# Optimization experiments

Measured on AMD Instinct MI355X. Metric: run time of the kernel, lower is better.

## Reference

```python
import jax, jax.numpy as jnp
import numpy as np

B, S, D_IN, D_ST = 4, 4096, 1024, 1024


def setup_inputs() -> dict:
    key = jax.random.key(0)
    ks = jax.random.split(key, 7)
    s_in = 1.0 / np.sqrt(D_IN)
    s_st = 1.0 / np.sqrt(D_ST)
    return {
        "x": jax.random.normal(ks[0], (B, S, D_IN), dtype=jnp.float32),
        "gate_w": jax.random.uniform(ks[1], (D_IN, D_ST), jnp.float32, -s_in, s_in),
        "gate_b": jax.random.uniform(ks[2], (D_ST,), jnp.float32, -s_in, s_in),
        "inp_w": jax.random.uniform(ks[3], (D_IN, D_ST), jnp.float32, -s_in, s_in),
        "inp_b": jax.random.uniform(ks[4], (D_ST,), jnp.float32, -s_in, s_in),
        "out_w": jax.random.uniform(ks[5], (D_ST, D_IN), jnp.float32, -s_st, s_st),
        "out_b": jax.random.uniform(ks[6], (D_IN,), jnp.float32, -s_st, s_st),
    }


def reference(x, gate_w, gate_b, inp_w, inp_b, out_w, out_b):
    # x: [B, S, D_in]
    inp = jnp.einsum("bsd,de->bse", x, inp_w) + inp_b      # [B,S,Dst]
    gate = jax.nn.sigmoid(jnp.einsum("bsd,de->bse", x, gate_w) + gate_b)
    b_t = (1.0 - gate) * inp                               # [B,S,Dst]

    # affine recurrence h_t = gate_t * h_{t-1} + b_t via lax.scan over time
    def step(h, ab):
        a, b = ab
        h = a * h + b
        return h, h

    a_sb = jnp.swapaxes(gate, 0, 1)  # [S,B,Dst]
    b_sb = jnp.swapaxes(b_t, 0, 1)
    h0 = jnp.zeros((x.shape[0], inp.shape[-1]), dtype=x.dtype)
    _, hs = jax.lax.scan(step, h0, (a_sb, b_sb))           # [S,B,Dst]
    scan_out = jnp.swapaxes(hs, 0, 1)                      # [B,S,Dst]

    return x + jnp.einsum("bse,ed->bsd", scan_out, out_w) + out_b
```

## Files before the change

### kernel.cpp

```cpp
#include <hip/hip_runtime.h>

typedef unsigned short u16;
typedef unsigned int   u32;
typedef __bf16 bf16x8 __attribute__((ext_vector_type(8)));
typedef float  f32x4  __attribute__((ext_vector_type(4)));

#define DEVI __device__ __forceinline__

DEVI u16 f2bf(float f) {
    union { float f; u32 u; } c; c.f = f;
    u32 u = c.u;
    u32 r = (u + 0x7fffu + ((u >> 16) & 1u)) >> 16;
    return (u16)r;
}
DEVI float bf2f(u16 v) {
    union { u32 u; float f; } c; c.u = ((u32)v) << 16;
    return c.f;
}

DEVI void gload16(const void* g, void* l) {
    __builtin_amdgcn_global_load_lds(
        (const __attribute__((address_space(1))) void*)g,
        (__attribute__((address_space(3))) void*)l, 16, 0, 0);
}


#define SP1     __builtin_amdgcn_s_setprio(1)
#define SP0     __builtin_amdgcn_s_setprio(0)

DEVI void stage_half(const u16* g, u16* slot, int tid) {
    const int r = tid >> 3;
    const int ks = (((tid & 7) ^ (r & 7)) << 3);
    gload16(g + (long)r * 1024 + ks, slot + tid * 8);
    gload16(g + (long)(r + 64) * 1024 + ks, slot + 4096 + tid * 8);
}

DEVI f32x4 mfma(const bf16x8& a, const bf16x8& b, const f32x4& c) {
    return __builtin_amdgcn_mfma_f32_16x16x32_bf16(a, b, c, 0, 0, 0);
}

#define PH2(Q, MB, READB, STG, GATE)                                         \
    {                                                                        \
        if (READB) {                                                         \
            _Pragma("unroll")                                                \
            for (int n = 0; n < 4; ++n) {                                    \
                bh[n][0] = *(const bf16x8*)(lds + (Q) + bbase + n * 1024 + kA); \
                bh[n][1] = *(const bf16x8*)(lds + (Q) + bbase + n * 1024 + kB); \
            }                                                                \
        }                                                                    \
        bf16x8 a0k0 = *(const bf16x8*)(lds + (Q) + abase + (MB) * 2048 + kA); \
        bf16x8 a0k1 = *(const bf16x8*)(lds + (Q) + abase + (MB) * 2048 + kB); \
        bf16x8 a1k0 = *(const bf16x8*)(lds + (Q) + abase + (MB) * 2048 + 1024 + kA); \
        bf16x8 a1k1 = *(const bf16x8*)(lds + (Q) + abase + (MB) * 2048 + 1024 + kB); \
        STG;                                                                 \
        SP1;                                                                 \
        _Pragma("unroll")                                                    \
        for (int n = 0; n < 4; ++n) {                                        \
            acc[(MB) * 2][n]     = mfma(a0k0, bh[n][0], acc[(MB) * 2][n]);   \
            acc[(MB) * 2][n]     = mfma(a0k1, bh[n][1], acc[(MB) * 2][n]);   \
            acc[(MB) * 2 + 1][n] = mfma(a1k0, bh[n][0], acc[(MB) * 2 + 1][n]); \
            acc[(MB) * 2 + 1][n] = mfma(a1k1, bh[n][1], acc[(MB) * 2 + 1][n]); \
        }                                                                    \
        {                                                                    \
            const int M2 = (MB) + 1;                                         \
            bf16x8 c0k0 = *(const bf16x8*)(lds + (Q) + abase + M2 * 2048 + kA); \
            bf16x8 c0k1 = *(const bf16x8*)(lds + (Q) + abase + M2 * 2048 + kB); \
            bf16x8 c1k0 = *(const bf16x8*)(lds + (Q) + abase + M2 * 2048 + 1024 + kA); \
            bf16x8 c1k1 = *(const bf16x8*)(lds + (Q) + abase + M2 * 2048 + 1024 + kB); \
            _Pragma("unroll")                                                \
            for (int n = 0; n < 4; ++n) {                                    \
                acc[M2 * 2][n]     = mfma(c0k0, bh[n][0], acc[M2 * 2][n]);   \
                acc[M2 * 2][n]     = mfma(c0k1, bh[n][1], acc[M2 * 2][n]);   \
                acc[M2 * 2 + 1][n] = mfma(c1k0, bh[n][0], acc[M2 * 2 + 1][n]); \
                acc[M2 * 2 + 1][n] = mfma(c1k1, bh[n][1], acc[M2 * 2 + 1][n]); \
            }                                                                \
        }                                                                    \
        SP0;                                                                 \
        GATE;                                                                \
    }

#define NOP do {} while (0)
#define TCLOSE { __syncthreads(); }
#define AH(t, h) (Ab + (long)(h) * 131072 + (t) * 64)
#define BH(t, h) (Bb + (long)(h) * 131072 + (t) * 64)

DEVI void pipe256(const u16* Ab, const u16* Bb, u16* lds,
                  f32x4 (&acc)[8][4], int tid) {
    const int lane = tid & 63;
    const int wm = (tid >> 6) >> 2, wn = (tid >> 6) & 3;
    const int kA = (((lane >> 4) ^ (lane & 7)) << 3);
    const int kB = kA ^ 32;
    const int abase = wm * 8192 + (lane & 15) * 64;
    const int bbase = 16384 + (wn >> 1) * 8192 + ((wn & 1) * 64 + (lane & 15)) * 64;

    stage_half(AH(0, 0), lds + 0,     tid);
    stage_half(AH(0, 1), lds + 8192,  tid);
    stage_half(BH(0, 0), lds + 16384, tid);
    stage_half(BH(0, 1), lds + 24576, tid);
    __syncthreads();

    bf16x8 bh[4][2];

#pragma unroll 1
    for (int j = 0; j < 7; ++j) {
        const int T = 2 * j;
        PH2(0, 0, 1,
            { stage_half(AH(T + 1, 0), lds + 32768, tid);
              stage_half(AH(T + 1, 1), lds + 32768 + 8192, tid); }, NOP);
        PH2(0, 2, 0,
            { stage_half(BH(T + 1, 0), lds + 32768 + 16384, tid);
              stage_half(BH(T + 1, 1), lds + 32768 + 24576, tid); }, TCLOSE);
        PH2(32768, 0, 1,
            { stage_half(AH(T + 2, 0), lds + 0, tid);
              stage_half(AH(T + 2, 1), lds + 8192, tid); }, NOP);
        PH2(32768, 2, 0,
            { stage_half(BH(T + 2, 0), lds + 16384, tid);
              stage_half(BH(T + 2, 1), lds + 24576, tid); }, TCLOSE);
    }
    PH2(0, 0, 1,
        { stage_half(AH(15, 0), lds + 32768, tid);
          stage_half(AH(15, 1), lds + 32768 + 8192, tid); }, NOP);
    PH2(0, 2, 0,
        { stage_half(BH(15, 0), lds + 32768 + 16384, tid);
          stage_half(BH(15, 1), lds + 32768 + 24576, tid); }, TCLOSE);
    PH2(32768, 0, 1, NOP, NOP);
    PH2(32768, 2, 0, NOP, NOP);
}


__global__ __launch_bounds__(512, 1) void k_gemm_cat8(
    const u16* __restrict__ A, const u16* __restrict__ Bcat,
    const float* __restrict__ gb, const float* __restrict__ ib,
    u32* __restrict__ ab, float2* __restrict__ cAB) {
    __shared__ __align__(16) u16 lds[65536];
    const int tid = threadIdx.x, lane = tid & 63;
    const int wm = (tid >> 6) >> 2, wn = (tid >> 6) & 3;

    int fid = (int)blockIdx.y * 8 + (int)blockIdx.x;
    int swz = (fid & 7) * 64 + (fid >> 3);
    const long bn = swz & 7, bm = swz >> 3;

    f32x4 acc[8][4] = {};
    pipe256(A + bm * 256 * 1024, Bcat + bn * 256 * 1024, lds, acc, tid);

    const long rbase = bm * 256 + wm * 128;
    const int chbase = (int)bn * 128 + wn * 32;
    float sA[2][8], sB[2][8];
#pragma unroll
    for (int t = 0; t < 2; ++t) {
        int ch = chbase + t * 16 + (lane & 15);
        float g0 = gb[ch], i0 = ib[ch];
#pragma unroll
        for (int m = 0; m < 8; ++m) {
            long row = rbase + m * 16 + ((lane >> 4) << 2);
            float Aseg = 1.0f, Bseg = 0.0f;
#pragma unroll
            for (int i = 0; i < 4; ++i) {
                float pg = acc[m][2 * t][i] + g0;
                float pi = acc[m][2 * t + 1][i] + i0;
                float aa = 1.0f / (1.0f + __expf(-pg));
                float bb = (1.0f - aa) * pi;
                u16 au = f2bf(aa), bu = f2bf(bb);
                ab[(row + i) * 1024 + ch] = (u32)au | ((u32)bu << 16);
                float ar = bf2f(au), br = bf2f(bu);
                Aseg = ar * Aseg;
                Bseg = ar * Bseg + br;
            }
            sA[t][m] = Aseg;
            sB[t][m] = Bseg;
        }
    }
#pragma unroll
    for (int t = 0; t < 2; ++t) {
#pragma unroll
        for (int c2 = 0; c2 < 2; ++c2) {
            float Ac = 1.0f, Bc = 0.0f;
#pragma unroll
            for (int mm = 0; mm < 4; ++mm) {
                int m = c2 * 4 + mm;
#pragma unroll
                for (int q = 0; q < 4; ++q) {
                    float Aq = __shfl(sA[t][m], (lane & 15) + q * 16);
                    float Bq = __shfl(sB[t][m], (lane & 15) + q * 16);
                    Ac = Aq * Ac;
                    Bc = Aq * Bc + Bq;
                }
            }
            if ((lane >> 4) == 0) {
                long gc = (rbase >> 6) + c2;
                int ch = chbase + t * 16 + (lane & 15);
                cAB[gc * 1024 + ch] = make_float2(Ac, Bc);
            }
        }
    }
}


__global__ __launch_bounds__(512, 1) void k_gemm_out8(
    const u16* __restrict__ A, const u16* __restrict__ Bt,
    const u16* __restrict__ xbf, const float* __restrict__ ob,
    float* __restrict__ out) {
    __shared__ __align__(16) u16 lds[65536];
    const int tid = threadIdx.x, lane = tid & 63;
    const int wm = (tid >> 6) >> 2, wn = (tid >> 6) & 3;

    int fid = (int)blockIdx.y * 4 + (int)blockIdx.x;
    int swz = (fid & 7) * 32 + (fid >> 3);
    const long bn = swz & 3, bm = swz >> 2;

    f32x4 acc[8][4] = {};
    pipe256(A + bm * 256 * 1024, Bt + bn * 256 * 1024, lds, acc, tid);

    const long rbase = bm * 256 + wm * 128;
    const int cbase = (int)bn * 256 + wn * 64;
#pragma unroll
    for (int n = 0; n < 4; ++n) {
        int col = cbase + n * 16 + (lane & 15);
        float o0 = ob[col];
#pragma unroll
        for (int m = 0; m < 8; ++m) {
            long row = rbase + m * 16 + ((lane >> 4) << 2);
#pragma unroll
            for (int i = 0; i < 4; ++i) {
                long o = (row + i) * 1024 + col;
                out[o] = acc[m][n][i] + o0 + bf2f(xbf[o]);
            }
        }
    }
}


__global__ __launch_bounds__(256) void k_prep(
    const float4* __restrict__ x4, uint2* __restrict__ xb2,
    const float* __restrict__ gw, const float* __restrict__ iw,
    u16* __restrict__ catW, const float* __restrict__ ow,
    u16* __restrict__ owT) {
    __shared__ float t[32][33];
    int bid = blockIdx.x;
    if (bid < 16384) {
        int i = bid * 256 + threadIdx.x;
        float4 v = x4[i];
        uint2 r;
        r.x = (u32)f2bf(v.x) | ((u32)f2bf(v.y) << 16);
        r.y = (u32)f2bf(v.z) | ((u32)f2bf(v.w) << 16);
        xb2[i] = r;
        return;
    }
    int xi = threadIdx.x & 31, y = threadIdx.x >> 5;
    if (bid < 18432) {
        int q = bid - 16384;
        int c0 = (q & 31) * 32, r0 = ((q >> 5) & 31) * 32, z = q >> 10;
        const float* w = z ? iw : gw;
        for (int i = y; i < 32; i += 8) t[i][xi] = w[(size_t)(r0 + i) * 1024 + c0 + xi];
        __syncthreads();
        for (int i = y; i < 32; i += 8) {
            int ch = c0 + i;
            int r = ((ch >> 4) << 5) | (z << 4) | (ch & 15);
            catW[(size_t)r * 1024 + r0 + xi] = f2bf(t[xi][i]);
        }
    } else {
        int q = bid - 18432;
        int c0 = (q & 31) * 32, r0 = (q >> 5) * 32;
        for (int i = y; i < 32; i += 8) t[i][xi] = ow[(size_t)(r0 + i) * 1024 + c0 + xi];
        __syncthreads();
        for (int i = y; i < 32; i += 8)
            owT[(size_t)(c0 + i) * 1024 + r0 + xi] = f2bf(t[xi][i]);
    }
}


__global__ __launch_bounds__(256) void k_scanB(const float2* __restrict__ cAB,
                                               float* __restrict__ hin) {
    int e = blockIdx.x * 256 + threadIdx.x;
    int bt = blockIdx.y;
    float H = 0.f;
#pragma unroll
    for (int c = 0; c < 64; ++c) {
        long s = ((long)bt * 64 + c) * 1024 + e;
        hin[s] = H;
        float2 v = cAB[s];
        H = v.x * H + v.y;
    }
}

__global__ __launch_bounds__(256) void k_scanC(const u32* __restrict__ ab,
                                               const float* __restrict__ hin,
                                               u16* __restrict__ hout) {
    int e = blockIdx.x * 256 + threadIdx.x;
    int c = blockIdx.y, bt = blockIdx.z;
    long base = ((long)bt * 4096 + c * 64) * 1024 + e;
    float H = hin[((long)bt * 64 + c) * 1024 + e];
#pragma unroll 4
    for (int i = 0; i < 64; ++i) {
        u32 v = ab[base + (long)i * 1024];
        H = bf2f((u16)v) * H + bf2f((u16)(v >> 16));
        hout[base + (long)i * 1024] = f2bf(H);
    }
}


extern "C" void kernel_launch(void* const* d_in, const int* in_sizes, int n_in,
                              void* d_out, int out_size, void* d_ws, size_t ws_size,
                              hipStream_t stream) {
    const float* x      = (const float*)d_in[0];
    const float* gate_w = (const float*)d_in[1];
    const float* gate_b = (const float*)d_in[2];
    const float* inp_w  = (const float*)d_in[3];
    const float* inp_b  = (const float*)d_in[4];
    const float* out_w  = (const float*)d_in[5];
    const float* out_b  = (const float*)d_in[6];
    float* out = (float*)d_out;

    const int Bsz = 4, S = 4096, Din = 1024, Dst = 1024;
    const int M = Bsz * S;

    char* w = (char*)d_ws;
    u16* xb      = (u16*)(w);
    u16* catW    = (u16*)(w + 33554432);
    u16* owT     = (u16*)(w + 37748736);
    u16* hbf     = (u16*)(w + 39845888);
    float2* cAB  = (float2*)(w + 73400320);
    float* hin   = (float*)(w + 75497472);

    u32* ab = (u32*)d_out;

    k_prep<<<19456, 256, 0, stream>>>((const float4*)x, (uint2*)xb,
                                      gate_w, inp_w, catW, out_w, owT);

    k_gemm_cat8<<<dim3(8, M / 256), 512, 0, stream>>>(xb, catW, gate_b, inp_b, ab, cAB);

    k_scanB<<<dim3(4, Bsz), 256, 0, stream>>>(cAB, hin);
    k_scanC<<<dim3(4, 64, Bsz), 256, 0, stream>>>(ab, hin, hbf);

    k_gemm_out8<<<dim3(4, M / 256), 512, 0, stream>>>(hbf, owT, xb, out_b, out);
}
```

Baseline: 165.5 us.

## Shrink GEMM tiles to 128x128 with 4 waves and two blocks per CU

Both GEMM kernels move from 256x256 tiles with 8 waves and one block per CU to 128x128 tiles with 4 waves and a launch bound of two blocks per CU. The LDS buffers are halved and the fine-grained phase interleaving is replaced by a simpler whole-tile double buffer. The grid becomes four times larger, which is meant to improve occupancy and wave balance and to let two resident blocks overlap each other's latency. In exchange each tile reuses its operands less, so more data is loaded from global memory and L2, and the carefully tuned intra-block pipelining is lost.

After: 162.4 us, median of 2. Within noise of the previous version (-1.9%).

```diff
diff --git a/kernel.cpp b/kernel.cpp
--- a/kernel.cpp
+++ b/kernel.cpp
@@ -28,130 +28,99 @@
 #define SP1     __builtin_amdgcn_s_setprio(1)
 #define SP0     __builtin_amdgcn_s_setprio(0)
 
-DEVI void stage_half(const u16* g, u16* slot, int tid) {
-    const int r = tid >> 3;
-    const int ks = (((tid & 7) ^ (r & 7)) << 3);
-    gload16(g + (long)r * 1024 + ks, slot + tid * 8);
-    gload16(g + (long)(r + 64) * 1024 + ks, slot + 4096 + tid * 8);
+DEVI void stage128(const u16* g, u16* slot, int tid) {
+    const int ks = (((tid & 7) ^ ((tid >> 3) & 7)) << 3);
+#pragma unroll
+    for (int j = 0; j < 4; ++j) {
+        const int r = j * 32 + (tid >> 3);
+        gload16(g + (long)r * 1024 + ks, slot + j * 2048 + tid * 8);
+    }
 }
 
 DEVI f32x4 mfma(const bf16x8& a, const bf16x8& b, const f32x4& c) {
     return __builtin_amdgcn_mfma_f32_16x16x32_bf16(a, b, c, 0, 0, 0);
 }
 
-#define PH2(Q, MB, READB, STG, GATE)                                         \
+#define NOP do {} while (0)
+#define TCLOSE { __syncthreads(); }
+
+#define TILE(Q, STG, SYNC)                                                   \
     {                                                                        \
-        if (READB) {                                                         \
+        STG;                                                                 \
+        bf16x8 bh0[4], bh1[4], aa0[4], aa1[4];                               \
+        _Pragma("unroll")                                                    \
+        for (int n = 0; n < 4; ++n) {                                        \
+            bh0[n] = *(const bf16x8*)(lds + (Q) + bbase + n * 1024 + kA);    \
+            bh1[n] = *(const bf16x8*)(lds + (Q) + bbase + n * 1024 + kB);    \
+        }                                                                    \
+        _Pragma("unroll")                                                    \
+        for (int m = 0; m < 4; ++m) {                                        \
+            aa0[m] = *(const bf16x8*)(lds + (Q) + abase + m * 1024 + kA);    \
+            aa1[m] = *(const bf16x8*)(lds + (Q) + abase + m * 1024 + kB);    \
+        }                                                                    \
+        SP1;                                                                 \
+        _Pragma("unroll")                                                    \
+        for (int m = 0; m < 4; ++m) {                                        \
             _Pragma("unroll")                                                \
             for (int n = 0; n < 4; ++n) {                                    \
-                bh[n][0] = *(const bf16x8*)(lds + (Q) + bbase + n * 1024 + kA); \
-                bh[n][1] = *(const bf16x8*)(lds + (Q) + bbase + n * 1024 + kB); \
-            }                                                                \
-        }                                                                    \
-        bf16x8 a0k0 = *(const bf16x8*)(lds + (Q) + abase + (MB) * 2048 + kA); \
-        bf16x8 a0k1 = *(const bf16x8*)(lds + (Q) + abase + (MB) * 2048 + kB); \
-        bf16x8 a1k0 = *(const bf16x8*)(lds + (Q) + abase + (MB) * 2048 + 1024 + kA); \
-        bf16x8 a1k1 = *(const bf16x8*)(lds + (Q) + abase + (MB) * 2048 + 1024 + kB); \
-        STG;                                                                 \
-        SP1;                                                                 \
-        _Pragma("unroll")                                                    \
-        for (int n = 0; n < 4; ++n) {                                        \
-            acc[(MB) * 2][n]     = mfma(a0k0, bh[n][0], acc[(MB) * 2][n]);   \
-            acc[(MB) * 2][n]     = mfma(a0k1, bh[n][1], acc[(MB) * 2][n]);   \
-            acc[(MB) * 2 + 1][n] = mfma(a1k0, bh[n][0], acc[(MB) * 2 + 1][n]); \
-            acc[(MB) * 2 + 1][n] = mfma(a1k1, bh[n][1], acc[(MB) * 2 + 1][n]); \
-        }                                                                    \
-        {                                                                    \
-            const int M2 = (MB) + 1;                                         \
-            bf16x8 c0k0 = *(const bf16x8*)(lds + (Q) + abase + M2 * 2048 + kA); \
-            bf16x8 c0k1 = *(const bf16x8*)(lds + (Q) + abase + M2 * 2048 + kB); \
-            bf16x8 c1k0 = *(const bf16x8*)(lds + (Q) + abase + M2 * 2048 + 1024 + kA); \
-            bf16x8 c1k1 = *(const bf16x8*)(lds + (Q) + abase + M2 * 2048 + 1024 + kB); \
-            _Pragma("unroll")                                                \
-            for (int n = 0; n < 4; ++n) {                                    \
-                acc[M2 * 2][n]     = mfma(c0k0, bh[n][0], acc[M2 * 2][n]);   \
-                acc[M2 * 2][n]     = mfma(c0k1, bh[n][1], acc[M2 * 2][n]);   \
-                acc[M2 * 2 + 1][n] = mfma(c1k0, bh[n][0], acc[M2 * 2 + 1][n]); \
-                acc[M2 * 2 + 1][n] = mfma(c1k1, bh[n][1], acc[M2 * 2 + 1][n]); \
+                acc[m][n] = mfma(aa0[m], bh0[n], acc[m][n]);                 \
+                acc[m][n] = mfma(aa1[m], bh1[n], acc[m][n]);                 \
             }                                                                \
         }                                                                    \
         SP0;                                                                 \
-        GATE;                                                                \
-    }
-
-#define NOP do {} while (0)
-#define TCLOSE { __syncthreads(); }
-#define AH(t, h) (Ab + (long)(h) * 131072 + (t) * 64)
-#define BH(t, h) (Bb + (long)(h) * 131072 + (t) * 64)
-
-DEVI void pipe256(const u16* Ab, const u16* Bb, u16* lds,
-                  f32x4 (&acc)[8][4], int tid) {
+        SYNC;                                                                \
+    }
+
+#define STA(t, buf) stage128(Ab + (t) * 64, lds + (buf), tid)
+#define STB(t, buf) stage128(Bb + (t) * 64, lds + (buf) + 8192, tid)
+
+DEVI void pipe128(const u16* Ab, const u16* Bb, u16* lds,
+                  f32x4 (&acc)[4][4], int tid) {
     const int lane = tid & 63;
-    const int wm = (tid >> 6) >> 2, wn = (tid >> 6) & 3;
+    const int wm = (tid >> 6) >> 1, wn = (tid >> 6) & 1;
     const int kA = (((lane >> 4) ^ (lane & 7)) << 3);
     const int kB = kA ^ 32;
-    const int abase = wm * 8192 + (lane & 15) * 64;
-    const int bbase = 16384 + (wn >> 1) * 8192 + ((wn & 1) * 64 + (lane & 15)) * 64;
-
-    stage_half(AH(0, 0), lds + 0,     tid);
-    stage_half(AH(0, 1), lds + 8192,  tid);
-    stage_half(BH(0, 0), lds + 16384, tid);
-    stage_half(BH(0, 1), lds + 24576, tid);
+    const int abase = wm * 4096 + (lane & 15) * 64;
+    const int bbase = 8192 + wn * 4096 + (lane & 15) * 64;
+
+    STA(0, 0); STB(0, 0);
     __syncthreads();
-
-    bf16x8 bh[4][2];
 
 #pragma unroll 1
     for (int j = 0; j < 7; ++j) {
         const int T = 2 * j;
-        PH2(0, 0, 1,
-            { stage_half(AH(T + 1, 0), lds + 32768, tid);
-              stage_half(AH(T + 1, 1), lds + 32768 + 8192, tid); }, NOP);
-        PH2(0, 2, 0,
-            { stage_half(BH(T + 1, 0), lds + 32768 + 16384, tid);
-              stage_half(BH(T + 1, 1), lds + 32768 + 24576, tid); }, TCLOSE);
-        PH2(32768, 0, 1,
-            { stage_half(AH(T + 2, 0), lds + 0, tid);
-              stage_half(AH(T + 2, 1), lds + 8192, tid); }, NOP);
-        PH2(32768, 2, 0,
-            { stage_half(BH(T + 2, 0), lds + 16384, tid);
-              stage_half(BH(T + 2, 1), lds + 24576, tid); }, TCLOSE);
-    }
-    PH2(0, 0, 1,
-        { stage_half(AH(15, 0), lds + 32768, tid);
-          stage_half(AH(15, 1), lds + 32768 + 8192, tid); }, NOP);
-    PH2(0, 2, 0,
-        { stage_half(BH(15, 0), lds + 32768 + 16384, tid);
-          stage_half(BH(15, 1), lds + 32768 + 24576, tid); }, TCLOSE);
-    PH2(32768, 0, 1, NOP, NOP);
-    PH2(32768, 2, 0, NOP, NOP);
-}
-
-
-__global__ __launch_bounds__(512, 1) void k_gemm_cat8(
+        TILE(0,     { STA(T + 1, 16384); STB(T + 1, 16384); }, TCLOSE);
+        TILE(16384, { STA(T + 2, 0);     STB(T + 2, 0);     }, TCLOSE);
+    }
+    TILE(0,     { STA(15, 16384); STB(15, 16384); }, TCLOSE);
+    TILE(16384, NOP, NOP);
+}
+
+
+__global__ __launch_bounds__(256, 2) void k_gemm_cat8(
     const u16* __restrict__ A, const u16* __restrict__ Bcat,
     const float* __restrict__ gb, const float* __restrict__ ib,
     u32* __restrict__ ab, float2* __restrict__ cAB) {
-    __shared__ __align__(16) u16 lds[65536];
+    __shared__ __align__(16) u16 lds[32768];
     const int tid = threadIdx.x, lane = tid & 63;
-    const int wm = (tid >> 6) >> 2, wn = (tid >> 6) & 3;
-
-    int fid = (int)blockIdx.y * 8 + (int)blockIdx.x;
-    int swz = (fid & 7) * 64 + (fid >> 3);
-    const long bn = swz & 7, bm = swz >> 3;
-
-    f32x4 acc[8][4] = {};
-    pipe256(A + bm * 256 * 1024, Bcat + bn * 256 * 1024, lds, acc, tid);
-
-    const long rbase = bm * 256 + wm * 128;
-    const int chbase = (int)bn * 128 + wn * 32;
-    float sA[2][8], sB[2][8];
+    const int wm = (tid >> 6) >> 1, wn = (tid >> 6) & 1;
+
+    int fid = (int)blockIdx.y * 16 + (int)blockIdx.x;
+    int swz = (fid & 7) * 256 + (fid >> 3);
+    const long bn = swz & 15, bm = swz >> 4;
+
+    f32x4 acc[4][4] = {};
+    pipe128(A + bm * 128 * 1024, Bcat + bn * 128 * 1024, lds, acc, tid);
+
+    const long rbase = bm * 128 + wm * 64;
+    const int chbase = (int)bn * 64 + wn * 32;
+    float sA[2][4], sB[2][4];
 #pragma unroll
     for (int t = 0; t < 2; ++t) {
         int ch = chbase + t * 16 + (lane & 15);
         float g0 = gb[ch], i0 = ib[ch];
 #pragma unroll
-        for (int m = 0; m < 8; ++m) {
+        for (int m = 0; m < 4; ++m) {
             long row = rbase + m * 16 + ((lane >> 4) << 2);
             float Aseg = 1.0f, Bseg = 0.0f;
 #pragma unroll
@@ -172,53 +141,49 @@
     }
 #pragma unroll
     for (int t = 0; t < 2; ++t) {
-#pragma unroll
-        for (int c2 = 0; c2 < 2; ++c2) {
-            float Ac = 1.0f, Bc = 0.0f;
-#pragma unroll
-            for (int mm = 0; mm < 4; ++mm) {
-                int m = c2 * 4 + mm;
-#pragma unroll
-                for (int q = 0; q < 4; ++q) {
-                    float Aq = __shfl(sA[t][m], (lane & 15) + q * 16);
-                    float Bq = __shfl(sB[t][m], (lane & 15) + q * 16);
-                    Ac = Aq * Ac;
-                    Bc = Aq * Bc + Bq;
-                }
+        float Ac = 1.0f, Bc = 0.0f;
+#pragma unroll
+        for (int m = 0; m < 4; ++m) {
+#pragma unroll
+            for (int q = 0; q < 4; ++q) {
+                float Aq = __shfl(sA[t][m], (lane & 15) + q * 16);
+                float Bq = __shfl(sB[t][m], (lane & 15) + q * 16);
+                Ac = Aq * Ac;
+                Bc = Aq * Bc + Bq;
             }
-            if ((lane >> 4) == 0) {
-                long gc = (rbase >> 6) + c2;
-                int ch = chbase + t * 16 + (lane & 15);
-                cAB[gc * 1024 + ch] = make_float2(Ac, Bc);
-            }
-        }
-    }
-}
-
-
-__global__ __launch_bounds__(512, 1) void k_gemm_out8(
+        }
+        if ((lane >> 4) == 0) {
+            long gc = rbase >> 6;
+            int ch = chbase + t * 16 + (lane & 15);
+            cAB[gc * 1024 + ch] = make_float2(Ac, Bc);
+        }
+    }
+}
+
+
+__global__ __launch_bounds__(256, 2) void k_gemm_out8(
     const u16* __restrict__ A, const u16* __restrict__ Bt,
     const u16* __restrict__ xbf, const float* __restrict__ ob,
     float* __restrict__ out) {
-    __shared__ __align__(16) u16 lds[65536];
+    __shared__ __align__(16) u16 lds[32768];
     const int tid = threadIdx.x, lane = tid & 63;
-    const int wm = (tid >> 6) >> 2, wn = (tid >> 6) & 3;
-
-    int fid = (int)blockIdx.y * 4 + (int)blockIdx.x;
-    int swz = (fid & 7) * 32 + (fid >> 3);
-    const long bn = swz & 3, bm = swz >> 2;
-
-    f32x4 acc[8][4] = {};
-    pipe256(A + bm * 256 * 1024, Bt + bn * 256 * 1024, lds, acc, tid);
-
-    const long rbase = bm * 256 + wm * 128;
-    const int cbase = (int)bn * 256 + wn * 64;
+    const int wm = (tid >> 6) >> 1, wn = (tid >> 6) & 1;
+
+    int fid = (int)blockIdx.y * 8 + (int)blockIdx.x;
+    int swz = (fid & 7) * 128 + (fid >> 3);
+    const long bn = swz & 7, bm = swz >> 3;
+
+    f32x4 acc[4][4] = {};
+    pipe128(A + bm * 128 * 1024, Bt + bn * 128 * 1024, lds, acc, tid);
+
+    const long rbase = bm * 128 + wm * 64;
+    const int cbase = (int)bn * 128 + wn * 64;
 #pragma unroll
     for (int n = 0; n < 4; ++n) {
         int col = cbase + n * 16 + (lane & 15);
         float o0 = ob[col];
 #pragma unroll
-        for (int m = 0; m < 8; ++m) {
+        for (int m = 0; m < 4; ++m) {
             long row = rbase + m * 16 + ((lane >> 4) << 2);
 #pragma unroll
             for (int i = 0; i < 4; ++i) {
@@ -327,10 +292,10 @@
     k_prep<<<19456, 256, 0, stream>>>((const float4*)x, (uint2*)xb,
                                       gate_w, inp_w, catW, out_w, owT);
 
-    k_gemm_cat8<<<dim3(8, M / 256), 512, 0, stream>>>(xb, catW, gate_b, inp_b, ab, cAB);
+    k_gemm_cat8<<<dim3(16, M / 128), 256, 0, stream>>>(xb, catW, gate_b, inp_b, ab, cAB);
 
     k_scanB<<<dim3(4, Bsz), 256, 0, stream>>>(cAB, hin);
     k_scanC<<<dim3(4, 64, Bsz), 256, 0, stream>>>(ab, hin, hbf);
 
-    k_gemm_out8<<<dim3(4, M / 256), 512, 0, stream>>>(hbf, owT, xb, out_b, out);
-}
+    k_gemm_out8<<<dim3(8, M / 128), 256, 0, stream>>>(hbf, owT, xb, out_b, out);
+}
```
